# Kernel optimization log

Hardware: AMD Instinct MI355X
Metric: run time of the kernel (lower is better)

## Reference

```python
import jax, jax.numpy as jnp
import numpy as np

T, N, F, S = 512, 64, 256, 1024  # seq_len, batch, behavior features, lstm size


def setup_inputs() -> dict:
    key = jax.random.key(0)
    k1, k2, k3 = jax.random.split(key, 3)
    x = jax.random.normal(k1, (T, N, F), dtype=jnp.float32)
    # stacked gate weights: order [i, f, g, o]
    Wx = jax.random.normal(k2, (4, F, S), dtype=jnp.float32) * 0.02
    Wh = jax.random.normal(k3, (4, S, S), dtype=jnp.float32) * 0.02
    b = jnp.zeros((4, S), dtype=jnp.float32)
    return {"x": x, "Wx": Wx, "Wh": Wh, "b": b}


def reference(x, Wx, Wh, b):
    # x: [T, n, f]; Wx: [4, f, s]; Wh: [4, s, s]; b: [4, s]
    n = x.shape[1]
    s = Wh.shape[-1]
    h0 = jnp.zeros((n, s), dtype=x.dtype)
    c0 = jnp.zeros((n, s), dtype=x.dtype)

    def step(carry, xt):
        h, c = carry
        # fused 4-gate projection: z[k] = xt @ Wx[k] + h @ Wh[k] + b[k]
        z = (jnp.einsum('nf,kfs->kns', xt, Wx)
             + jnp.einsum('ns,kst->knt', h, Wh)
             + b[:, None, :])  # [4, n, s]
        i = jax.nn.sigmoid(z[0])
        f = jax.nn.sigmoid(z[1])
        g = jnp.tanh(z[2])
        o = jax.nn.sigmoid(z[3])
        c = f * c + i * g
        h = o * jnp.tanh(c)
        return (h, c), h

    (_, _), hs = jax.lax.scan(step, (h0, c0), x)
    return hs  # [T, n, s]
```

## Files before the change

### kernel.cpp

```cpp
#include <hip/hip_runtime.h>
#include <hip/hip_bf16.h>

#define T_LEN 512
#define NB 64
#define FB 256
#define SB 1024
#define NWG 256

typedef __attribute__((ext_vector_type(8))) short bf16x8;
typedef __attribute__((ext_vector_type(4))) float f32x4;
typedef __attribute__((ext_vector_type(2))) float f32x2;

#define MFMA(a, b, c) __builtin_amdgcn_mfma_f32_16x16x32_bf16((a), (b), (c), 0, 0, 0)

__device__ __forceinline__ bf16x8 load_frag_dev(const __hip_bfloat16* p) {
    const unsigned long long* q = (const unsigned long long*)p;
    unsigned long long a = __hip_atomic_load(q,     __ATOMIC_RELAXED, __HIP_MEMORY_SCOPE_AGENT);
    unsigned long long b = __hip_atomic_load(q + 1, __ATOMIC_RELAXED, __HIP_MEMORY_SCOPE_AGENT);
    union { unsigned long long u[2]; bf16x8 v; } r;
    r.u[0] = a; r.u[1] = b;
    return r.v;
}

__global__ void xfrag_kernel(const float* __restrict__ x, __hip_bfloat16* __restrict__ xaf) {
    int tid  = blockIdx.x * 256 + threadIdx.x;
    int l    = tid & 63;
    int frag = tid >> 6;
    int kc   = frag & 7;
    int m    = (frag >> 3) & 3;
    int t    = frag >> 5;
    int row  = m * 16 + (l & 15);
    int k0   = kc * 32 + 8 * (l >> 4);
    const float* src = x + ((size_t)(t * NB + row)) * FB + k0;
    __hip_bfloat16* dst = xaf + (size_t)frag * 512 + l * 8;
#pragma unroll
    for (int e = 0; e < 8; ++e) dst[e] = __float2bfloat16(src[e]);
}

__global__ void wfrag_kernel(const float* __restrict__ Wx, const float* __restrict__ Wh,
                             __hip_bfloat16* __restrict__ wbf) {
    int tid  = blockIdx.x * 256 + threadIdx.x;
    int l    = tid & 63;
    int frag = tid >> 6;
    int g    = frag & 3;
    int kcw  = (frag >> 2) % 10;
    int wv   = (frag / 40) & 3;
    int sb   = frag / 160;
    int kc   = (kcw < 2) ? (wv * 2 + kcw) : (8 + wv * 8 + (kcw - 2));
    int s    = sb * 16 + (l & 15);
    int k0   = kc * 32 + 8 * (l >> 4);
    __hip_bfloat16* dst = wbf + (size_t)frag * 512 + l * 8;
#pragma unroll
    for (int e = 0; e < 8; ++e) {
        int k = k0 + e;
        float v = (k < FB) ? Wx[((size_t)g * FB + k) * SB + s]
                           : Wh[((size_t)g * SB + (k - FB)) * SB + s];
        dst[e] = __float2bfloat16(v);
    }
}

__global__ __launch_bounds__(256, 1) void lstm_persist(
    const __hip_bfloat16* __restrict__ xaf,
    const __hip_bfloat16* __restrict__ wbf,
    const float* __restrict__ bias,
    __hip_bfloat16* __restrict__ hfrag,
    float* __restrict__ cbuf,
    float* __restrict__ out,
    unsigned int* __restrict__ flag,
    int t0, int nsteps, int use_sync)
{
    __shared__ float part[4 * 16 * 4 * 17];
    const int tid = threadIdx.x;
    const int wv  = tid >> 6;
    const int l   = tid & 63;
    const int ng  = blockIdx.x >> 6;
    const int sb  = blockIdx.x & 63;
    const int lr  = l & 15;
    const int lg  = l >> 4;

    const int fidx = (ng * 64 + wv * 16 + (l & 15)) * 2;

    const int gact = (tid < 128);
    const int gn   = (tid >> 3) & 15;
    const int sc0  = (tid & 7) * 2;

    bf16x8 wf[40];
    {
        const __hip_bfloat16* wp = wbf + ((size_t)(sb * 4 + wv) * 40) * 512 + l * 8;
#pragma unroll
        for (int i = 0; i < 40; ++i) wf[i] = *reinterpret_cast<const bf16x8*>(wp + (size_t)i * 512);
    }
    float br[8];
    f32x2 creg = {0.f, 0.f};
    if (gact) {
#pragma unroll
        for (int g = 0; g < 4; ++g) {
            br[g * 2]     = bias[g * SB + sb * 16 + sc0];
            br[g * 2 + 1] = bias[g * SB + sb * 16 + sc0 + 1];
        }
        creg = *reinterpret_cast<const f32x2*>(
            &cbuf[(ng * 16 + gn) * SB + sb * 16 + sc0]);
    }

    f32x4 acc[4];
#pragma unroll
    for (int g = 0; g < 4; ++g) acc[g] = (f32x4){0.f, 0.f, 0.f, 0.f};
    {
        const __hip_bfloat16* xs = xaf + (size_t)t0 * 16384;
#pragma unroll
        for (int j = 0; j < 2; ++j) {
            int kc = wv * 2 + j;
            bf16x8 a = *reinterpret_cast<const bf16x8*>(xs + (size_t)(ng * 8 + kc) * 512 + l * 8);
#pragma unroll
            for (int g = 0; g < 4; ++g) acc[g] = MFMA(a, wf[j * 4 + g], acc[g]);
        }
    }

    for (int tt = 0; tt < nsteps; ++tt) {
        const int t = t0 + tt;

        if (use_sync && tt > 0) {
            unsigned lic = 1u;
            const unsigned int* s3 = flag + (size_t)(t - 3) * 512;
            if (tt > 2)
                lic = __hip_atomic_load(&s3[(ng * 64 + l) * 2], __ATOMIC_RELAXED, __HIP_MEMORY_SCOPE_AGENT);
            const unsigned int* f1 = flag + (size_t)(t - 1) * 512;
            for (;;) {
                unsigned a = __hip_atomic_load(&f1[fidx], __ATOMIC_RELAXED, __HIP_MEMORY_SCOPE_AGENT);
                if (__all(a != 0)) break;
            }
            if (tt > 2) {
                while (!__all(lic != 0))
                    lic = __hip_atomic_load(&s3[(ng * 64 + l) * 2], __ATOMIC_RELAXED, __HIP_MEMORY_SCOPE_AGENT);
            }
            asm volatile("" ::: "memory");
        }

        const __hip_bfloat16* hs = hfrag + (size_t)(t & 3) * 65536;
#pragma unroll
        for (int j = 0; j < 8; ++j) {
            int kch = wv * 8 + j;
            bf16x8 a = load_frag_dev(hs + (size_t)(kch * 4 + ng) * 512 + l * 8);
#pragma unroll
            for (int g = 0; g < 4; ++g) acc[g] = MFMA(a, wf[(2 + j) * 4 + g], acc[g]);
        }

#pragma unroll
        for (int g = 0; g < 4; ++g)
#pragma unroll
            for (int i = 0; i < 4; ++i)
                part[((wv * 16 + lg * 4 + i) * 4 + g) * 17 + lr] = acc[g][i];
        __syncthreads();

        if (gact) {
            float z[4][2];
#pragma unroll
            for (int g = 0; g < 4; ++g) {
                float s0 = 0.f, s1 = 0.f;
#pragma unroll
                for (int w2 = 0; w2 < 4; ++w2) {
                    const float* pr = &part[((w2 * 16 + gn) * 4 + g) * 17 + sc0];
                    s0 += pr[0];
                    s1 += pr[1];
                }
                z[g][0] = s0 + br[g * 2];
                z[g][1] = s1 + br[g * 2 + 1];
            }
            float hv[2];
#pragma unroll
            for (int e = 0; e < 2; ++e) {
                float ig = 1.f / (1.f + expf(-z[0][e]));
                float fg = 1.f / (1.f + expf(-z[1][e]));
                float gg = tanhf(z[2][e]);
                float og = 1.f / (1.f + expf(-z[3][e]));
                float c  = fg * creg[e] + ig * gg;
                hv[e]    = og * tanhf(c);
                creg[e]  = c;
            }
            int sg0 = sb * 16 + sc0;
            *reinterpret_cast<f32x2*>(&out[(size_t)t * (NB * SB) + (size_t)(ng * 16 + gn) * SB + sg0])
                = (f32x2){hv[0], hv[1]};
            unsigned u0 = (unsigned)__bfloat16_as_ushort(__float2bfloat16(hv[0]));
            unsigned u1 = (unsigned)__bfloat16_as_ushort(__float2bfloat16(hv[1]));
            int kch  = sg0 >> 5;
            int k8   = sg0 & 31;
            int lane = (k8 >> 3) * 16 + gn;
            unsigned int* hd = reinterpret_cast<unsigned int*>(
                hfrag + (size_t)((t + 1) & 3) * 65536
                + (size_t)(kch * 4 + ng) * 512 + lane * 8 + (k8 & 7));
            __hip_atomic_store(hd, u0 | (u1 << 16), __ATOMIC_RELAXED, __HIP_MEMORY_SCOPE_AGENT);
        }

        if (use_sync) {
            __syncthreads();
            if (tid == 0)
                __hip_atomic_store(&flag[((size_t)t * 256 + blockIdx.x) * 2], 1u,
                                   __ATOMIC_RELAXED, __HIP_MEMORY_SCOPE_AGENT);
        }

        if (tt + 1 < nsteps) {
#pragma unroll
            for (int g = 0; g < 4; ++g) acc[g] = (f32x4){0.f, 0.f, 0.f, 0.f};
            const __hip_bfloat16* xs = xaf + (size_t)(t + 1) * 16384;
#pragma unroll
            for (int j = 0; j < 2; ++j) {
                int kc = wv * 2 + j;
                bf16x8 a = *reinterpret_cast<const bf16x8*>(xs + (size_t)(ng * 8 + kc) * 512 + l * 8);
#pragma unroll
                for (int g = 0; g < 4; ++g) acc[g] = MFMA(a, wf[j * 4 + g], acc[g]);
            }
        }
    }

    if (gact)
        *reinterpret_cast<f32x2*>(&cbuf[(ng * 16 + gn) * SB + sb * 16 + sc0]) = creg;
}

extern "C" void kernel_launch(void* const* d_in, const int* in_sizes, int n_in,
                              void* d_out, int out_size, void* d_ws, size_t ws_size,
                              hipStream_t stream) {
    const float* x  = (const float*)d_in[0];
    const float* Wx = (const float*)d_in[1];
    const float* Wh = (const float*)d_in[2];
    const float* b  = (const float*)d_in[3];
    float* out = (float*)d_out;

    char* ws = (char*)d_ws;
    __hip_bfloat16* xaf   = (__hip_bfloat16*)ws;
    __hip_bfloat16* wbf   = (__hip_bfloat16*)(ws + 16777216);
    __hip_bfloat16* hfrag = (__hip_bfloat16*)(ws + 27262976);
    float*          cbuf  = (float*)(ws + 27787264);
    unsigned int*   flag  = (unsigned int*)(ws + 28049408);

    hipLaunchKernelGGL(xfrag_kernel, dim3(4096), dim3(256), 0, stream, x, xaf);
    hipLaunchKernelGGL(wfrag_kernel, dim3(2560), dim3(256), 0, stream, Wx, Wh, wbf);
    hipMemsetAsync(hfrag, 0, 524288, stream);
    hipMemsetAsync(cbuf, 0, 262144, stream);
    hipMemsetAsync(flag, 0, 1048576, stream);

    const __hip_bfloat16* p_xaf = xaf;
    const __hip_bfloat16* p_wbf = wbf;
    const float* p_bias = b;
    __hip_bfloat16* p_hfrag = hfrag;
    float* p_cbuf = cbuf;
    float* p_out = out;
    unsigned int* p_flag = flag;
    int z0 = 0, ns = T_LEN, us = 1;
    void* args[] = {&p_xaf, &p_wbf, &p_bias, &p_hfrag, &p_cbuf, &p_out, &p_flag, &z0, &ns, &us};
    hipError_t err = hipLaunchCooperativeKernel((void*)lstm_persist, dim3(NWG), dim3(256),
                                                args, 0, stream);
    if (err != hipSuccess) {
        for (int t = 0; t < T_LEN; ++t) {
            hipLaunchKernelGGL(lstm_persist, dim3(NWG), dim3(256), 0, stream,
                               xaf, wbf, b, hfrag, cbuf, out, flag, t, 1, 0);
        }
    }
}
```

Before: 1.568 ms.

## Replace t-3 flag wait with NaN-sentinel validation of h fragments

Drops the wait on the step t-3 flags and the post-epilogue block barrier. The consumer now keeps re-reading its h fragments until none of them holds the NaN sentinel, and a second wave re-arms the slot for step t+3 with sentinels. The epilogue moves from 128 threads doing 2 columns each to one wave doing 4 columns with 64-bit h stores. Partial sums are double-buffered in LDS with padding, and the flag is set right after the h store instead of after a __syncthreads. The step t-1 flag spin is still kept. This shortens the per-step critical path but relies on relaxed atomics ordering, and a real h value equal to the sentinel bit pattern would stall the loop.

```diff
diff --git a/kernel.cpp b/kernel.cpp
--- a/kernel.cpp
+++ b/kernel.cpp
@@ -7,20 +7,13 @@
 #define SB 1024
 #define NWG 256
 
+#define SENT32 0x7FC07FC0u
+#define SENT64 0x7FC07FC07FC07FC0ULL
+
 typedef __attribute__((ext_vector_type(8))) short bf16x8;
 typedef __attribute__((ext_vector_type(4))) float f32x4;
-typedef __attribute__((ext_vector_type(2))) float f32x2;
 
 #define MFMA(a, b, c) __builtin_amdgcn_mfma_f32_16x16x32_bf16((a), (b), (c), 0, 0, 0)
-
-__device__ __forceinline__ bf16x8 load_frag_dev(const __hip_bfloat16* p) {
-    const unsigned long long* q = (const unsigned long long*)p;
-    unsigned long long a = __hip_atomic_load(q,     __ATOMIC_RELAXED, __HIP_MEMORY_SCOPE_AGENT);
-    unsigned long long b = __hip_atomic_load(q + 1, __ATOMIC_RELAXED, __HIP_MEMORY_SCOPE_AGENT);
-    union { unsigned long long u[2]; bf16x8 v; } r;
-    r.u[0] = a; r.u[1] = b;
-    return r.v;
-}
 
 __global__ void xfrag_kernel(const float* __restrict__ x, __hip_bfloat16* __restrict__ xaf) {
     int tid  = blockIdx.x * 256 + threadIdx.x;
@@ -59,6 +52,10 @@
     }
 }
 
+__global__ void sentinit_kernel(unsigned int* __restrict__ p) {
+    p[blockIdx.x * 256 + threadIdx.x] = SENT32;
+}
+
 __global__ __launch_bounds__(256, 1) void lstm_persist(
     const __hip_bfloat16* __restrict__ xaf,
     const __hip_bfloat16* __restrict__ wbf,
@@ -67,9 +64,9 @@
     float* __restrict__ cbuf,
     float* __restrict__ out,
     unsigned int* __restrict__ flag,
-    int t0, int nsteps, int use_sync)
+    int t0, int nsteps)
 {
-    __shared__ float part[4 * 16 * 4 * 17];
+    __shared__ float part[2][4 * 16 * 4 * 20];
     const int tid = threadIdx.x;
     const int wv  = tid >> 6;
     const int l   = tid & 63;
@@ -80,9 +77,8 @@
 
     const int fidx = (ng * 64 + wv * 16 + (l & 15)) * 2;
 
-    const int gact = (tid < 128);
-    const int gn   = (tid >> 3) & 15;
-    const int sc0  = (tid & 7) * 2;
+    const int gn4 = l >> 2;
+    const int scq = (l & 3) * 4;
 
     bf16x8 wf[40];
     {
@@ -90,16 +86,13 @@
 #pragma unroll
         for (int i = 0; i < 40; ++i) wf[i] = *reinterpret_cast<const bf16x8*>(wp + (size_t)i * 512);
     }
-    float br[8];
-    f32x2 creg = {0.f, 0.f};
-    if (gact) {
-#pragma unroll
-        for (int g = 0; g < 4; ++g) {
-            br[g * 2]     = bias[g * SB + sb * 16 + sc0];
-            br[g * 2 + 1] = bias[g * SB + sb * 16 + sc0 + 1];
-        }
-        creg = *reinterpret_cast<const f32x2*>(
-            &cbuf[(ng * 16 + gn) * SB + sb * 16 + sc0]);
+    f32x4 brv[4];
+    f32x4 creg = {0.f, 0.f, 0.f, 0.f};
+    if (wv == 0) {
+#pragma unroll
+        for (int g = 0; g < 4; ++g)
+            brv[g] = *reinterpret_cast<const f32x4*>(&bias[g * SB + sb * 16 + scq]);
+        creg = *reinterpret_cast<const f32x4*>(&cbuf[(ng * 16 + gn4) * SB + sb * 16 + scq]);
     }
 
     f32x4 acc[4];
@@ -117,85 +110,97 @@
     }
 
     for (int tt = 0; tt < nsteps; ++tt) {
-        const int t = t0 + tt;
-
-        if (use_sync && tt > 0) {
-            unsigned lic = 1u;
-            const unsigned int* s3 = flag + (size_t)(t - 3) * 512;
-            if (tt > 2)
-                lic = __hip_atomic_load(&s3[(ng * 64 + l) * 2], __ATOMIC_RELAXED, __HIP_MEMORY_SCOPE_AGENT);
+        const int t  = t0 + tt;
+        const int pb = t & 1;
+
+        if (tt > 0) {
             const unsigned int* f1 = flag + (size_t)(t - 1) * 512;
             for (;;) {
                 unsigned a = __hip_atomic_load(&f1[fidx], __ATOMIC_RELAXED, __HIP_MEMORY_SCOPE_AGENT);
                 if (__all(a != 0)) break;
             }
-            if (tt > 2) {
-                while (!__all(lic != 0))
-                    lic = __hip_atomic_load(&s3[(ng * 64 + l) * 2], __ATOMIC_RELAXED, __HIP_MEMORY_SCOPE_AGENT);
-            }
             asm volatile("" ::: "memory");
         }
 
         const __hip_bfloat16* hs = hfrag + (size_t)(t & 3) * 65536;
+        unsigned long long v[16];
+        for (;;) {
+#pragma unroll
+            for (int j = 0; j < 8; ++j) {
+                const unsigned long long* q = reinterpret_cast<const unsigned long long*>(
+                    hs + (size_t)((wv * 8 + j) * 4 + ng) * 512 + l * 8);
+                v[2 * j]     = __hip_atomic_load(q,     __ATOMIC_RELAXED, __HIP_MEMORY_SCOPE_AGENT);
+                v[2 * j + 1] = __hip_atomic_load(q + 1, __ATOMIC_RELAXED, __HIP_MEMORY_SCOPE_AGENT);
+            }
+            bool ok = true;
+#pragma unroll
+            for (int k = 0; k < 16; ++k) {
+                unsigned lo = (unsigned)v[k], hi = (unsigned)(v[k] >> 32);
+                ok = ok && (lo != SENT32) && (hi != SENT32);
+            }
+            if (__all(ok)) break;
+        }
+        asm volatile("" ::: "memory");
+
 #pragma unroll
         for (int j = 0; j < 8; ++j) {
-            int kch = wv * 8 + j;
-            bf16x8 a = load_frag_dev(hs + (size_t)(kch * 4 + ng) * 512 + l * 8);
-#pragma unroll
-            for (int g = 0; g < 4; ++g) acc[g] = MFMA(a, wf[(2 + j) * 4 + g], acc[g]);
+            union { unsigned long long u[2]; bf16x8 a; } ua;
+            ua.u[0] = v[2 * j];
+            ua.u[1] = v[2 * j + 1];
+#pragma unroll
+            for (int g = 0; g < 4; ++g) acc[g] = MFMA(ua.a, wf[(2 + j) * 4 + g], acc[g]);
         }
 
 #pragma unroll
         for (int g = 0; g < 4; ++g)
 #pragma unroll
             for (int i = 0; i < 4; ++i)
-                part[((wv * 16 + lg * 4 + i) * 4 + g) * 17 + lr] = acc[g][i];
+                part[pb][((wv * 16 + lg * 4 + i) * 4 + g) * 20 + lr] = acc[g][i];
         __syncthreads();
 
-        if (gact) {
-            float z[4][2];
+        if (wv == 0) {
+            f32x4 z[4];
 #pragma unroll
             for (int g = 0; g < 4; ++g) {
-                float s0 = 0.f, s1 = 0.f;
-#pragma unroll
-                for (int w2 = 0; w2 < 4; ++w2) {
-                    const float* pr = &part[((w2 * 16 + gn) * 4 + g) * 17 + sc0];
-                    s0 += pr[0];
-                    s1 += pr[1];
-                }
-                z[g][0] = s0 + br[g * 2];
-                z[g][1] = s1 + br[g * 2 + 1];
-            }
-            float hv[2];
-#pragma unroll
-            for (int e = 0; e < 2; ++e) {
+                f32x4 s = {0.f, 0.f, 0.f, 0.f};
+#pragma unroll
+                for (int w2 = 0; w2 < 4; ++w2)
+                    s += *reinterpret_cast<const f32x4*>(
+                        &part[pb][((w2 * 16 + gn4) * 4 + g) * 20 + scq]);
+                z[g] = s + brv[g];
+            }
+            float hv[4];
+            unsigned long long hu = 0;
+#pragma unroll
+            for (int e = 0; e < 4; ++e) {
                 float ig = 1.f / (1.f + expf(-z[0][e]));
                 float fg = 1.f / (1.f + expf(-z[1][e]));
                 float gg = tanhf(z[2][e]);
                 float og = 1.f / (1.f + expf(-z[3][e]));
                 float c  = fg * creg[e] + ig * gg;
-                hv[e]    = og * tanhf(c);
+                float h  = og * tanhf(c);
                 creg[e]  = c;
-            }
-            int sg0 = sb * 16 + sc0;
-            *reinterpret_cast<f32x2*>(&out[(size_t)t * (NB * SB) + (size_t)(ng * 16 + gn) * SB + sg0])
-                = (f32x2){hv[0], hv[1]};
-            unsigned u0 = (unsigned)__bfloat16_as_ushort(__float2bfloat16(hv[0]));
-            unsigned u1 = (unsigned)__bfloat16_as_ushort(__float2bfloat16(hv[1]));
-            int kch  = sg0 >> 5;
-            int k8   = sg0 & 31;
-            int lane = (k8 >> 3) * 16 + gn;
-            unsigned int* hd = reinterpret_cast<unsigned int*>(
+                hv[e]    = h;
+                hu |= (unsigned long long)__bfloat16_as_ushort(__float2bfloat16(h)) << (16 * e);
+            }
+            int k8hi = 2 * (sb & 1) + ((l & 3) >> 1);
+            int lane = k8hi * 16 + gn4;
+            unsigned long long* hd = reinterpret_cast<unsigned long long*>(
                 hfrag + (size_t)((t + 1) & 3) * 65536
-                + (size_t)(kch * 4 + ng) * 512 + lane * 8 + (k8 & 7));
-            __hip_atomic_store(hd, u0 | (u1 << 16), __ATOMIC_RELAXED, __HIP_MEMORY_SCOPE_AGENT);
-        }
-
-        if (use_sync) {
-            __syncthreads();
-            if (tid == 0)
+                + (size_t)((sb >> 1) * 4 + ng) * 512 + lane * 8) + ((l & 3) & 1);
+            __hip_atomic_store(hd, hu, __ATOMIC_RELAXED, __HIP_MEMORY_SCOPE_AGENT);
+            asm volatile("" ::: "memory");
+            if (l == 0)
                 __hip_atomic_store(&flag[((size_t)t * 256 + blockIdx.x) * 2], 1u,
                                    __ATOMIC_RELAXED, __HIP_MEMORY_SCOPE_AGENT);
+            *reinterpret_cast<f32x4*>(
+                &out[(size_t)t * (NB * SB) + (size_t)(ng * 16 + gn4) * SB + sb * 16 + scq])
+                = (f32x4){hv[0], hv[1], hv[2], hv[3]};
+        } else if (wv == 1) {
+            unsigned long long* sp = reinterpret_cast<unsigned long long*>(
+                hfrag + (size_t)((t + 3) & 3) * 65536)
+                + (size_t)((sb >> 1) * 4 + ng) * 128 + (sb & 1) * 64 + l;
+            __hip_atomic_store(sp, SENT64, __ATOMIC_RELAXED, __HIP_MEMORY_SCOPE_AGENT);
         }
 
         if (tt + 1 < nsteps) {
@@ -212,8 +217,8 @@
         }
     }
 
-    if (gact)
-        *reinterpret_cast<f32x2*>(&cbuf[(ng * 16 + gn) * SB + sb * 16 + sc0]) = creg;
+    if (wv == 0)
+        *reinterpret_cast<f32x4*>(&cbuf[(ng * 16 + gn4) * SB + sb * 16 + scq]) = creg;
 }
 
 extern "C" void kernel_launch(void* const* d_in, const int* in_sizes, int n_in,
@@ -234,7 +239,9 @@
 
     hipLaunchKernelGGL(xfrag_kernel, dim3(4096), dim3(256), 0, stream, x, xaf);
     hipLaunchKernelGGL(wfrag_kernel, dim3(2560), dim3(256), 0, stream, Wx, Wh, wbf);
-    hipMemsetAsync(hfrag, 0, 524288, stream);
+    hipMemsetAsync(hfrag, 0, 131072, stream);
+    hipLaunchKernelGGL(sentinit_kernel, dim3(384), dim3(256), 0, stream,
+                       (unsigned int*)(hfrag + 65536));
     hipMemsetAsync(cbuf, 0, 262144, stream);
     hipMemsetAsync(flag, 0, 1048576, stream);
 
@@ -245,14 +252,14 @@
     float* p_cbuf = cbuf;
     float* p_out = out;
     unsigned int* p_flag = flag;
-    int z0 = 0, ns = T_LEN, us = 1;
-    void* args[] = {&p_xaf, &p_wbf, &p_bias, &p_hfrag, &p_cbuf, &p_out, &p_flag, &z0, &ns, &us};
+    int z0 = 0, ns = T_LEN;
+    void* args[] = {&p_xaf, &p_wbf, &p_bias, &p_hfrag, &p_cbuf, &p_out, &p_flag, &z0, &ns};
     hipError_t err = hipLaunchCooperativeKernel((void*)lstm_persist, dim3(NWG), dim3(256),
                                                 args, 0, stream);
     if (err != hipSuccess) {
         for (int t = 0; t < T_LEN; ++t) {
             hipLaunchKernelGGL(lstm_persist, dim3(NWG), dim3(256), 0, stream,
-                               xaf, wbf, b, hfrag, cbuf, out, flag, t, 1, 0);
-        }
-    }
-}
+                               xaf, wbf, b, hfrag, cbuf, out, flag, t, 1);
+        }
+    }
+}
```

Result: slower. 2.452 ms (+56.3%).
